# Kernel tuning notes

Hardware: AMD Instinct MI355X
Metric: run time of the kernel (lower is better)

The kernel has to match this reference:

```python
import jax, jax.numpy as jnp
import numpy as np

B, L, D = 8, 2048, 1024


def setup_inputs() -> dict:
    key = jax.random.key(0)
    kq, kk, kv, km, kw1, kb1, kw2, kb2 = jax.random.split(key, 8)
    q = jax.random.normal(kq, (B, L, D), dtype=jnp.float32)
    k = jax.random.normal(kk, (B, L, D), dtype=jnp.float32)
    v = jax.random.normal(kv, (B, L, D), dtype=jnp.float32)
    attn_mask = jax.random.randint(km, (B, L, L), 0, 2).astype(bool)
    # nn.Linear(d_model, 1) params (Kaiming-uniform-ish scale)
    bound = 1.0 / np.sqrt(D)
    W1 = jax.random.uniform(kw1, (D, 1), minval=-bound, maxval=bound, dtype=jnp.float32)
    b1 = jax.random.uniform(kb1, (1,), minval=-bound, maxval=bound, dtype=jnp.float32)
    W2 = jax.random.uniform(kw2, (D, 1), minval=-bound, maxval=bound, dtype=jnp.float32)
    b2 = jax.random.uniform(kb2, (1,), minval=-bound, maxval=bound, dtype=jnp.float32)
    return {"q": q, "k": k, "v": v, "attn_mask": attn_mask,
            "W1": W1, "b1": b1, "W2": W2, "b2": b2}


def reference(q, k, v, attn_mask, W1, b1, W2, b2):
    # linear-to-scalar projections (dropout is identity in eval mode)
    q_s = (q @ W1 + b1)[..., 0]          # [B, L]
    k_s = (k @ W2 + b2)[..., 0]          # [B, L]
    # additive (concat) attention scores via broadcast add -> [B, L, L]
    attn = q_s[:, :, None] + k_s[:, None, :]
    attn = jnp.where(attn_mask, -jnp.inf, attn)
    attn = jax.nn.softmax(attn, axis=-1)
    attn = jnp.where(attn_mask, jnp.float32(0.0), attn)
    out = jnp.einsum('bls,bsd->bld', attn, v)  # bmm(attn, v)
    return out, attn
```

## Files before the change

### kernel.cpp

```cpp
#include <hip/hip_runtime.h>
#include <hip/hip_bf16.h>

#define B 8
#define L 2048
#define D 1024

typedef __bf16 bf16x8 __attribute__((ext_vector_type(8)));
typedef __bf16 bf16x4 __attribute__((ext_vector_type(4)));
typedef float f32x4 __attribute__((ext_vector_type(4)));

__global__ __launch_bounds__(256) void proj_kernel(const float* __restrict__ k,
                                                   const float* __restrict__ W2,
                                                   const float* __restrict__ b2,
                                                   float* __restrict__ ks) {
    int row = blockIdx.x;
    int t = threadIdx.x;
    const float4* k4 = (const float4*)(k + (size_t)row * D);
    const float4* w4 = (const float4*)W2;
    float4 a = k4[t];
    float4 w = w4[t];
    float p = a.x * w.x + a.y * w.y + a.z * w.z + a.w * w.w;
    for (int off = 32; off > 0; off >>= 1)
        p += __shfl_down(p, off, 64);
    __shared__ float red[4];
    int wid = t >> 6, lane = t & 63;
    if (lane == 0) red[wid] = p;
    __syncthreads();
    if (t == 0) {
        ks[row] = red[0] + red[1] + red[2] + red[3] + b2[0];
    }
}

__global__ __launch_bounds__(256) void exp_kernel(const float* __restrict__ ks,
                                                  float* __restrict__ e) {
    int b = blockIdx.x;
    int t = threadIdx.x;
    const float* row = ks + (size_t)b * L;
    float m = -1e30f;
    for (int j = t; j < L; j += 256) m = fmaxf(m, row[j]);
    for (int off = 32; off > 0; off >>= 1)
        m = fmaxf(m, __shfl_down(m, off, 64));
    __shared__ float red[4];
    __shared__ float mb;
    int wid = t >> 6, lane = t & 63;
    if (lane == 0) red[wid] = m;
    __syncthreads();
    if (t == 0) mb = fmaxf(fmaxf(red[0], red[1]), fmaxf(red[2], red[3]));
    __syncthreads();
    float mm = mb;
    float* eo = e + (size_t)b * L;
    for (int j = t; j < L; j += 256) eo[j] = expf(row[j] - mm);
}

__global__ __launch_bounds__(256) void transpose_v(const float* __restrict__ v,
                                                   __bf16* __restrict__ vT) {
    __shared__ float tile[32][33];
    int b = blockIdx.z;
    int j0 = blockIdx.y * 32;
    int d0 = blockIdx.x * 32;
    int t = threadIdx.x;
    int jl = t >> 3;
    int dl = (t & 7) * 4;
    float4 val = *(const float4*)(v + ((size_t)b * L + j0 + jl) * D + d0 + dl);
    tile[jl][dl + 0] = val.x;
    tile[jl][dl + 1] = val.y;
    tile[jl][dl + 2] = val.z;
    tile[jl][dl + 3] = val.w;
    __syncthreads();
    int dl2 = t >> 3;
    int jl2 = (t & 7) * 4;
    bf16x4 o;
    o[0] = (__bf16)tile[jl2 + 0][dl2];
    o[1] = (__bf16)tile[jl2 + 1][dl2];
    o[2] = (__bf16)tile[jl2 + 2][dl2];
    o[3] = (__bf16)tile[jl2 + 3][dl2];
    *(bf16x4*)(vT + ((size_t)b * D + d0 + dl2) * L + j0 + jl2) = o;
}

__global__ __launch_bounds__(256) void row_kernel(const int* __restrict__ mask,
                                                  const float* __restrict__ e,
                                                  float* __restrict__ attn,
                                                  __bf16* __restrict__ P) {
    __shared__ float w[L];
    __shared__ float red[4];
    __shared__ float zsh;
    int bid = blockIdx.x;
    int b = bid >> 11;
    int t = threadIdx.x;
    const int4* m4 = (const int4*)(mask + (size_t)bid * L);
    const float4* e4 = (const float4*)(e + (size_t)b * L);
    float z = 0.f;
#pragma unroll
    for (int c = 0; c < 2; c++) {
        int idx = t * 2 + c;
        int4 mm = m4[idx];
        float4 ee = e4[idx];
        float4 ww;
        ww.x = mm.x ? 0.f : ee.x;
        ww.y = mm.y ? 0.f : ee.y;
        ww.z = mm.z ? 0.f : ee.z;
        ww.w = mm.w ? 0.f : ee.w;
        *(float4*)&w[idx * 4] = ww;
        z += ww.x + ww.y + ww.z + ww.w;
    }
    for (int off = 32; off > 0; off >>= 1)
        z += __shfl_down(z, off, 64);
    int wid = t >> 6, lane = t & 63;
    if (lane == 0) red[wid] = z;
    __syncthreads();
    if (t == 0) zsh = 1.f / (red[0] + red[1] + red[2] + red[3]);
    __syncthreads();
    float invZ = zsh;
    float4* a4 = (float4*)(attn + (size_t)bid * L);
    __bf16* prow = P + (size_t)bid * L;
#pragma unroll
    for (int c = 0; c < 2; c++) {
        int idx = t * 2 + c;
        float4 ww = *(float4*)&w[idx * 4];
        float4 aa;
        aa.x = ww.x * invZ;
        aa.y = ww.y * invZ;
        aa.z = ww.z * invZ;
        aa.w = ww.w * invZ;
        a4[idx] = aa;
        bf16x4 pp;
        pp[0] = (__bf16)aa.x;
        pp[1] = (__bf16)aa.y;
        pp[2] = (__bf16)aa.z;
        pp[3] = (__bf16)aa.w;
        *(bf16x4*)(prow + idx * 4) = pp;
    }
}

#define BM 128
#define BN 128
#define BK 32
#define LDA 40

__global__ __launch_bounds__(256) void gemm_kernel(const __bf16* __restrict__ P,
                                                   const __bf16* __restrict__ vT,
                                                   float* __restrict__ out) {
    __shared__ __bf16 As[BM][LDA];
    __shared__ __bf16 Bs[BN][LDA];
    int b = blockIdx.z;
    int i0 = blockIdx.x * BM;
    int d0 = blockIdx.y * BN;
    int t = threadIdx.x;
    int wave = t >> 6, lane = t & 63;
    int wr = wave >> 1, wc = wave & 1;
    const __bf16* Ab = P + ((size_t)b * L + i0) * L;
    const __bf16* Bb = vT + ((size_t)b * D + d0) * L;

    f32x4 acc[4][4];
#pragma unroll
    for (int ti = 0; ti < 4; ti++)
#pragma unroll
        for (int tj = 0; tj < 4; tj++)
            acc[ti][tj] = (f32x4){0.f, 0.f, 0.f, 0.f};

    int lrow = lane & 15;
    int koff = (lane >> 4) * 8;

    for (int k0 = 0; k0 < L; k0 += BK) {
        __syncthreads();
#pragma unroll
        for (int s = 0; s < 2; s++) {
            int c = t + s * 256;
            int row = c >> 2;
            int off = (c & 3) * 8;
            bf16x8 va = *(const bf16x8*)(Ab + (size_t)row * L + k0 + off);
            *(bf16x8*)&As[row][off] = va;
            bf16x8 vb = *(const bf16x8*)(Bb + (size_t)row * L + k0 + off);
            *(bf16x8*)&Bs[row][off] = vb;
        }
        __syncthreads();

        bf16x8 af[4], bfr[4];
#pragma unroll
        for (int ti = 0; ti < 4; ti++)
            af[ti] = *(const bf16x8*)&As[wr * 64 + ti * 16 + lrow][koff];
#pragma unroll
        for (int tj = 0; tj < 4; tj++)
            bfr[tj] = *(const bf16x8*)&Bs[wc * 64 + tj * 16 + lrow][koff];
#pragma unroll
        for (int ti = 0; ti < 4; ti++)
#pragma unroll
            for (int tj = 0; tj < 4; tj++)
                acc[ti][tj] = __builtin_amdgcn_mfma_f32_16x16x32_bf16(
                    af[ti], bfr[tj], acc[ti][tj], 0, 0, 0);
    }

    int col = lane & 15;
    int rquad = (lane >> 4) * 4;
#pragma unroll
    for (int ti = 0; ti < 4; ti++) {
#pragma unroll
        for (int tj = 0; tj < 4; tj++) {
#pragma unroll
            for (int r = 0; r < 4; r++) {
                int row = i0 + wr * 64 + ti * 16 + rquad + r;
                int c2 = d0 + wc * 64 + tj * 16 + col;
                out[((size_t)b * L + row) * D + c2] = acc[ti][tj][r];
            }
        }
    }
}

extern "C" void kernel_launch(void* const* d_in, const int* in_sizes, int n_in,
                              void* d_out, int out_size, void* d_ws, size_t ws_size,
                              hipStream_t stream) {
    const float* k = (const float*)d_in[1];
    const float* v = (const float*)d_in[2];
    const int* mask = (const int*)d_in[3];
    const float* W2 = (const float*)d_in[6];
    const float* b2 = (const float*)d_in[7];

    float* out = (float*)d_out;
    float* attn = out + (size_t)B * L * D;

    char* wp = (char*)d_ws;
    float* ks = (float*)wp;            wp += (size_t)B * L * 4;
    float* e = (float*)wp;             wp += (size_t)B * L * 4;
    __bf16* vT = (__bf16*)wp;          wp += (size_t)B * D * L * 2;
    __bf16* P = (__bf16*)wp;           wp += (size_t)B * L * L * 2;

    proj_kernel<<<B * L, 256, 0, stream>>>(k, W2, b2, ks);
    exp_kernel<<<B, 256, 0, stream>>>(ks, e);
    transpose_v<<<dim3(D / 32, L / 32, B), 256, 0, stream>>>(v, vT);
    row_kernel<<<B * L, 256, 0, stream>>>(mask, e, attn, P);
    gemm_kernel<<<dim3(L / BM, D / BN, B), 256, 0, stream>>>(P, vT, out);
}
```

Measured before the change: 544.1 us.

## Use direct global-to-LDS loads in GEMM and streamline projection and row kernels

The GEMM tile loads now use the global_load_lds builtin to write global memory straight into LDS, bypassing registers, and the LDS padding is dropped so the layout matches the wave-contiguous 16-byte-per-lane writes. The projection kernel gives each wave its own row, removing the shared-memory reduction and barrier. The row kernel keeps masked exponentials in registers instead of an LDS buffer and uses strided, coalesced indexing. Dropping the LDS padding may bring back bank conflicts on the MFMA fragment reads.

```diff
diff --git a/kernel.cpp b/kernel.cpp
--- a/kernel.cpp
+++ b/kernel.cpp
@@ -8,27 +8,29 @@
 typedef __bf16 bf16x8 __attribute__((ext_vector_type(8)));
 typedef __bf16 bf16x4 __attribute__((ext_vector_type(4)));
 typedef float f32x4 __attribute__((ext_vector_type(4)));
+
+typedef __attribute__((address_space(3))) char lds_char;
+typedef const __attribute__((address_space(1))) char glob_char;
 
 __global__ __launch_bounds__(256) void proj_kernel(const float* __restrict__ k,
                                                    const float* __restrict__ W2,
                                                    const float* __restrict__ b2,
                                                    float* __restrict__ ks) {
-    int row = blockIdx.x;
-    int t = threadIdx.x;
+    int t = threadIdx.x;
+    int wave = t >> 6, lane = t & 63;
+    int row = blockIdx.x * 4 + wave;
     const float4* k4 = (const float4*)(k + (size_t)row * D);
     const float4* w4 = (const float4*)W2;
-    float4 a = k4[t];
-    float4 w = w4[t];
-    float p = a.x * w.x + a.y * w.y + a.z * w.z + a.w * w.w;
+    float p = 0.f;
+#pragma unroll
+    for (int s = 0; s < 4; s++) {
+        float4 a = k4[s * 64 + lane];
+        float4 w = w4[s * 64 + lane];
+        p += a.x * w.x + a.y * w.y + a.z * w.z + a.w * w.w;
+    }
     for (int off = 32; off > 0; off >>= 1)
         p += __shfl_down(p, off, 64);
-    __shared__ float red[4];
-    int wid = t >> 6, lane = t & 63;
-    if (lane == 0) red[wid] = p;
-    __syncthreads();
-    if (t == 0) {
-        ks[row] = red[0] + red[1] + red[2] + red[3] + b2[0];
-    }
+    if (lane == 0) ks[row] = p + b2[0];
 }
 
 __global__ __launch_bounds__(256) void exp_kernel(const float* __restrict__ ks,
@@ -81,7 +83,6 @@
                                                   const float* __restrict__ e,
                                                   float* __restrict__ attn,
                                                   __bf16* __restrict__ P) {
-    __shared__ float w[L];
     __shared__ float red[4];
     __shared__ float zsh;
     int bid = blockIdx.x;
@@ -89,10 +90,11 @@
     int t = threadIdx.x;
     const int4* m4 = (const int4*)(mask + (size_t)bid * L);
     const float4* e4 = (const float4*)(e + (size_t)b * L);
+    float4 wv[2];
     float z = 0.f;
 #pragma unroll
-    for (int c = 0; c < 2; c++) {
-        int idx = t * 2 + c;
+    for (int s = 0; s < 2; s++) {
+        int idx = s * 256 + t;
         int4 mm = m4[idx];
         float4 ee = e4[idx];
         float4 ww;
@@ -100,7 +102,7 @@
         ww.y = mm.y ? 0.f : ee.y;
         ww.z = mm.z ? 0.f : ee.z;
         ww.w = mm.w ? 0.f : ee.w;
-        *(float4*)&w[idx * 4] = ww;
+        wv[s] = ww;
         z += ww.x + ww.y + ww.z + ww.w;
     }
     for (int off = 32; off > 0; off >>= 1)
@@ -114,14 +116,13 @@
     float4* a4 = (float4*)(attn + (size_t)bid * L);
     __bf16* prow = P + (size_t)bid * L;
 #pragma unroll
-    for (int c = 0; c < 2; c++) {
-        int idx = t * 2 + c;
-        float4 ww = *(float4*)&w[idx * 4];
+    for (int s = 0; s < 2; s++) {
+        int idx = s * 256 + t;
         float4 aa;
-        aa.x = ww.x * invZ;
-        aa.y = ww.y * invZ;
-        aa.z = ww.z * invZ;
-        aa.w = ww.w * invZ;
+        aa.x = wv[s].x * invZ;
+        aa.y = wv[s].y * invZ;
+        aa.z = wv[s].z * invZ;
+        aa.w = wv[s].w * invZ;
         a4[idx] = aa;
         bf16x4 pp;
         pp[0] = (__bf16)aa.x;
@@ -135,13 +136,12 @@
 #define BM 128
 #define BN 128
 #define BK 32
-#define LDA 40
 
 __global__ __launch_bounds__(256) void gemm_kernel(const __bf16* __restrict__ P,
                                                    const __bf16* __restrict__ vT,
                                                    float* __restrict__ out) {
-    __shared__ __bf16 As[BM][LDA];
-    __shared__ __bf16 Bs[BN][LDA];
+    __shared__ __bf16 As[BM][BK];
+    __shared__ __bf16 Bs[BN][BK];
     int b = blockIdx.z;
     int i0 = blockIdx.x * BM;
     int d0 = blockIdx.y * BN;
@@ -165,13 +165,18 @@
         __syncthreads();
 #pragma unroll
         for (int s = 0; s < 2; s++) {
-            int c = t + s * 256;
-            int row = c >> 2;
+            int cbase = s * 256 + wave * 64;
+            int c = cbase + lane;
+            int r = c >> 2;
             int off = (c & 3) * 8;
-            bf16x8 va = *(const bf16x8*)(Ab + (size_t)row * L + k0 + off);
-            *(bf16x8*)&As[row][off] = va;
-            bf16x8 vb = *(const bf16x8*)(Bb + (size_t)row * L + k0 + off);
-            *(bf16x8*)&Bs[row][off] = vb;
+            const __bf16* ga = Ab + (size_t)r * L + k0 + off;
+            __builtin_amdgcn_global_load_lds((glob_char*)ga,
+                                             (lds_char*)((char*)As + cbase * 16),
+                                             16, 0, 0);
+            const __bf16* gb = Bb + (size_t)r * L + k0 + off;
+            __builtin_amdgcn_global_load_lds((glob_char*)gb,
+                                             (lds_char*)((char*)Bs + cbase * 16),
+                                             16, 0, 0);
         }
         __syncthreads();
 
@@ -224,7 +229,7 @@
     __bf16* vT = (__bf16*)wp;          wp += (size_t)B * D * L * 2;
     __bf16* P = (__bf16*)wp;           wp += (size_t)B * L * L * 2;
 
-    proj_kernel<<<B * L, 256, 0, stream>>>(k, W2, b2, ks);
+    proj_kernel<<<B * L / 4, 256, 0, stream>>>(k, W2, b2, ks);
     exp_kernel<<<B, 256, 0, stream>>>(ks, e);
     transpose_v<<<dim3(D / 32, L / 32, B), 256, 0, stream>>>(v, vT);
     row_kernel<<<B * L, 256, 0, stream>>>(mask, e, attn, P);
```

Result: no change. 541.2 us (-0.5%).
